# Kernel tuning notes

Measured on AMD Instinct MI355X. Metric: run time of the kernel, lower is better.

## Reference

```python
import jax, jax.numpy as jnp
import numpy as np
import math

HEAD_DIM = 64
RP_DIM = 256
B, H, N = 4, 8, 4096
EPS = 1e-4  # performer positive-feature epsilon


def _ortho_gaussian_matrix(m, d, seed=0):
    # gaussian_orthogonal_random_matrix, scaling=0: stack QR-orthogonalized
    # d x d gaussian blocks, scale rows by norms of an iid gaussian matrix.
    rng = np.random.default_rng(seed)
    blocks = []
    for _ in range(int(np.ceil(m / d))):
        g = rng.standard_normal((d, d))
        q, _ = np.linalg.qr(g)
        blocks.append(q.T)
    mat = np.concatenate(blocks, axis=0)[:m]
    multiplier = np.linalg.norm(rng.standard_normal((m, d)), axis=1)
    return (multiplier[:, None] * mat).astype(np.float32)


def _softmax_features(x, proj, is_query):
    # FAVOR+ positive random features: ratio * exp(Wx - ||x||^2/2 - stab) + eps
    ratio = proj.shape[0] ** -0.5
    xp = jnp.einsum('bhnd,md->bhnm', x, proj)
    diag = 0.5 * jnp.sum(x * x, axis=-1, keepdims=True)
    if is_query:
        stab = jnp.max(xp, axis=-1, keepdims=True)
    else:
        stab = jnp.max(xp, axis=(-1, -2), keepdims=True)
    return ratio * (jnp.exp(xp - diag - stab) + EPS)


def setup_inputs() -> dict:
    key = jax.random.key(0)
    kq, kk, kv = jax.random.split(key, 3)
    Q = jax.random.normal(kq, (B, H, N, HEAD_DIM), dtype=jnp.float32)
    K = jax.random.normal(kk, (B, H, N, HEAD_DIM), dtype=jnp.float32)
    V = jax.random.normal(kv, (B, H, N, HEAD_DIM), dtype=jnp.float32)
    mask = jnp.ones((B, N), dtype=jnp.float32)
    projection = jnp.asarray(_ortho_gaussian_matrix(RP_DIM, HEAD_DIM, seed=0))
    return {'Q': Q, 'K': K, 'V': V, 'mask': mask, 'projection': projection}


def reference(Q, K, V, mask, projection):
    scale = HEAD_DIM ** -0.25  # 1/sqrt(sqrt(head_dim))
    m = mask[:, None, :, None]
    q = Q * scale
    k = K * scale * m
    v = V * m
    phi_q = _softmax_features(q, projection, is_query=True)   # [b,h,n,m]
    phi_k = _softmax_features(k, projection, is_query=False)  # [b,h,n,m]
    # non-causal linear attention
    k_sum = jnp.sum(phi_k, axis=2)                                   # [b,h,m]
    D_inv = 1.0 / jnp.einsum('bhnm,bhm->bhn', phi_q, k_sum)          # [b,h,n]
    context = jnp.einsum('bhnm,bhne->bhme', phi_k, v)                # [b,h,m,e]
    out = jnp.einsum('bhme,bhnm,bhn->bhne', context, phi_q, D_inv)   # [b,h,n,e]
    return out
```

## Files before the change

kernel.cpp:

```cpp
#include <hip/hip_runtime.h>
#include <hip/hip_bf16.h>


typedef __attribute__((ext_vector_type(8))) short short8;
typedef __attribute__((ext_vector_type(4))) float floatx4;

constexpr int BB = 4, HH = 8, NN = 4096, DD = 64, MM = 256, BH = 32;
constexpr int NCH = 16;
constexpr float SCALE = 0.3535533905932738f;
constexpr float RATIO = 0.0625f;
constexpr float EPSI  = 1e-4f;
constexpr float NEGINF = -3.4e38f;

__device__ inline unsigned pk2(float a, float b) {
  unsigned ua = __float_as_uint(a) + 0x8000u;
  unsigned ub = __float_as_uint(b) + 0x8000u;
  return (ua >> 16) | (ub & 0xffff0000u);
}
__device__ inline float hif(float x) {
  return __uint_as_float((__float_as_uint(x) + 0x8000u) & 0xffff0000u);
}
__device__ inline unsigned short bhi(float x) {
  return (unsigned short)((__float_as_uint(x) + 0x8000u) >> 16);
}
__device__ inline int ph16(int i) { return (i & 56) | ((i + (i >> 3)) & 7); }

union Frag { short8 s8; unsigned u[4]; };

__device__ inline void atomicMaxF(float* a, float v) {
  unsigned* ai = (unsigned*)a;
  unsigned old = __atomic_load_n(ai, __ATOMIC_RELAXED);
  while (__uint_as_float(old) < v) {
    unsigned assumed = old;
    old = atomicCAS(ai, assumed, __float_as_uint(v));
    if (old == assumed) break;
  }
}

__global__ __launch_bounds__(256) void prep_kernel(
    const float* __restrict__ proj, unsigned short* __restrict__ projH,
    unsigned short* __restrict__ projL, float* __restrict__ stabk,
    float* __restrict__ Vs, float* __restrict__ ctxsum,
    float* __restrict__ ksE) {
  const int i = blockIdx.x * 256 + threadIdx.x;
  float v = proj[i];
  projH[i] = bhi(v);
  projL[i] = bhi(v - hif(v));
  if (i < BH) stabk[i] = NEGINF;
  if (i < 2048) { Vs[i] = 0.f; ctxsum[i] = 0.f; }
  if (i < 8192) ksE[i] = 0.f;
}

template <bool PARTIAL>
__global__ __launch_bounds__(256) void kside_kernel(
    const float* __restrict__ K, const float* __restrict__ V,
    const float* __restrict__ mask,
    const unsigned short* __restrict__ projH, const unsigned short* __restrict__ projL,
    float* __restrict__ stabk, float* __restrict__ ksE,
    float* __restrict__ ctxOut, float* __restrict__ Vs) {
  const int bh = blockIdx.y, b = bh >> 3;
  const int t = threadIdx.x;
  const int w = t >> 6, l = t & 63, c = l & 15, sq = l >> 4;
  const int m0 = w * 64;

  __shared__ __align__(16) unsigned short sK[2][32 * 72];
  __shared__ __align__(16) unsigned short sVt[2][64 * 40];
  __shared__ float sDiag[32];
  __shared__ float sRed[4];
  __shared__ float sVsum[4][64];
  __shared__ __align__(16) unsigned short sPhi[4][2][512];

  Frag Bp[4][2][2];
#pragma unroll
  for (int tt = 0; tt < 4; ++tt)
#pragma unroll
    for (int s = 0; s < 2; ++s) {
      const size_t o = (size_t)(m0 + tt * 16 + c) * DD + s * 32 + sq * 8;
      Bp[tt][s][0].s8 = *(const short8*)&projH[o];
      Bp[tt][s][1].s8 = *(const short8*)&projL[o];
    }

  floatx4 ctxacc[4][4];
#pragma unroll
  for (int i = 0; i < 4; ++i)
#pragma unroll
    for (int j = 0; j < 4; ++j) ctxacc[i][j] = (floatx4){0.f, 0.f, 0.f, 0.f};
  float ksac[4] = {0.f, 0.f, 0.f, 0.f};
  float mxloc = NEGINF;
  float vsacc = 0.f;

  const int r0 = blockIdx.x * 256;

  float4 pk4[2], pv4[2];
  float pmk[2], pmv[2];
  {
    const int rb = r0;
#pragma unroll
    for (int rep = 0; rep < 2; ++rep) {
      const int f = t + rep * 256;
      const int n = f >> 4;
      pmk[rep] = mask[b * NN + rb + n];
      pk4[rep] = *(const float4*)(K + ((size_t)bh * NN + rb + n) * DD + (f & 15) * 4);
      const int n_loc = w * 4 + rep * 16 + sq;
      pmv[rep] = mask[b * NN + rb + n_loc];
      pv4[rep] = *(const float4*)(V + ((size_t)bh * NN + rb + n_loc) * DD + c * 4);
    }
  }

  for (int ch = 0; ch < 8; ++ch) {
    __syncthreads();

#pragma unroll
    for (int rep = 0; rep < 2; ++rep) {
      const int f = t + rep * 256;
      const int n = f >> 4, dg = f & 15;
      const float msc = pmk[rep] * SCALE;
      float k0 = pk4[rep].x * msc, k1 = pk4[rep].y * msc,
            k2 = pk4[rep].z * msc, k3 = pk4[rep].w * msc;
      float ss = fmaf(k0, k0, fmaf(k1, k1, fmaf(k2, k2, k3 * k3)));
      ss += __shfl_xor(ss, 1); ss += __shfl_xor(ss, 2);
      ss += __shfl_xor(ss, 4); ss += __shfl_xor(ss, 8);
      if (dg == 0) sDiag[n] = 0.5f * ss;
      unsigned h0 = pk2(k0, k1), h1 = pk2(k2, k3);
      float q0 = k0 - hif(k0), q1 = k1 - hif(k1);
      float q2 = k2 - hif(k2), q3 = k3 - hif(k3);
      *(uint2*)(&sK[0][n * 72 + dg * 4]) = make_uint2(h0, h1);
      *(uint2*)(&sK[1][n * 72 + dg * 4]) = make_uint2(pk2(q0, q1), pk2(q2, q3));
    }

#pragma unroll
    for (int rep = 0; rep < 2; ++rep) {
      const int nb = w * 4 + rep * 16;
      const float mk = pmv[rep];
      float4 vv = pv4[rep];
      float va[4] = {vv.x * mk, vv.y * mk, vv.z * mk, vv.w * mk};
      float g[4];
#pragma unroll
      for (int k = 0; k < 4; ++k) {
        const int gi = (sq + k) & 3;
        float sel = va[(sq - k) & 3];
        g[gi] = __shfl(sel, gi * 16 + c);
      }
      const int estar = c * 4 + sq;
      vsacc += ((g[0] + g[1]) + (g[2] + g[3]));
      unsigned h0 = pk2(g[0], g[1]), h1 = pk2(g[2], g[3]);
      float q0 = g[0] - hif(g[0]), q1 = g[1] - hif(g[1]);
      float q2 = g[2] - hif(g[2]), q3 = g[3] - hif(g[3]);
      *(uint2*)(&sVt[0][estar * 40 + nb]) = make_uint2(h0, h1);
      *(uint2*)(&sVt[1][estar * 40 + nb]) = make_uint2(pk2(q0, q1), pk2(q2, q3));
    }
    __syncthreads();

    if (ch < 7) {
      const int rb = r0 + (ch + 1) * 32;
#pragma unroll
      for (int rep = 0; rep < 2; ++rep) {
        const int f = t + rep * 256;
        const int n = f >> 4;
        pmk[rep] = mask[b * NN + rb + n];
        pk4[rep] = *(const float4*)(K + ((size_t)bh * NN + rb + n) * DD + (f & 15) * 4);
        const int n_loc = w * 4 + rep * 16 + sq;
        pmv[rep] = mask[b * NN + rb + n_loc];
        pv4[rep] = *(const float4*)(V + ((size_t)bh * NN + rb + n_loc) * DD + c * 4);
      }
    }

    Frag Ak[2][2][2];
#pragma unroll
    for (int i = 0; i < 2; ++i)
#pragma unroll
      for (int s = 0; s < 2; ++s) {
        Ak[i][s][0].s8 = *(const short8*)&sK[0][(i * 16 + c) * 72 + s * 32 + sq * 8];
        Ak[i][s][1].s8 = *(const short8*)&sK[1][(i * 16 + c) * 72 + s * 32 + sq * 8];
      }
    Frag Bv[4][2];
#pragma unroll
    for (int E = 0; E < 4; ++E) {
      Bv[E][0].s8 = *(const short8*)&sVt[0][(E * 16 + c) * 40 + sq * 8];
      Bv[E][1].s8 = *(const short8*)&sVt[1][(E * 16 + c) * 40 + sq * 8];
    }

#pragma unroll
    for (int tt = 0; tt < 4; ++tt) {
      floatx4 xacc[2];
#pragma unroll
      for (int i = 0; i < 2; ++i) {
        floatx4 a = (floatx4){0.f, 0.f, 0.f, 0.f};
#pragma unroll
        for (int s = 0; s < 2; ++s) {
          a = __builtin_amdgcn_mfma_f32_16x16x32_bf16(Ak[i][s][0].s8, Bp[tt][s][0].s8, a, 0, 0, 0);
          a = __builtin_amdgcn_mfma_f32_16x16x32_bf16(Ak[i][s][0].s8, Bp[tt][s][1].s8, a, 0, 0, 0);
          a = __builtin_amdgcn_mfma_f32_16x16x32_bf16(Ak[i][s][1].s8, Bp[tt][s][0].s8, a, 0, 0, 0);
        }
        xacc[i] = a;
      }
      const int qp_c = sq >> 1, half = (sq & 1) * 4;
#pragma unroll
      for (int i = 0; i < 2; ++i) {
        float p[4];
#pragma unroll
        for (int jj = 0; jj < 4; ++jj) {
          float xp = xacc[i][jj];
          mxloc = fmaxf(mxloc, xp);
          p[jj] = __expf(xp - sDiag[i * 16 + sq * 4 + jj]);
          ksac[tt] += p[jj];
        }
        unsigned h0 = pk2(p[0], p[1]), h1 = pk2(p[2], p[3]);
        float q0 = p[0] - hif(p[0]), q1 = p[1] - hif(p[1]);
        float q2 = p[2] - hif(p[2]), q3 = p[3] - hif(p[3]);
        const int tl = (i * 2 + qp_c) * 16 + c;
        const int idx = ph16(tl) * 8 + half;
        *(uint2*)&sPhi[w][0][idx] = make_uint2(h0, h1);
        *(uint2*)&sPhi[w][1][idx] = make_uint2(pk2(q0, q1), pk2(q2, q3));
      }
      Frag Ap[2];
      Ap[0].s8 = *(const short8*)&sPhi[w][0][ph16(l) * 8];
      Ap[1].s8 = *(const short8*)&sPhi[w][1][ph16(l) * 8];
#pragma unroll
      for (int E = 0; E < 4; ++E) {
        ctxacc[tt][E] = __builtin_amdgcn_mfma_f32_16x16x32_bf16(Ap[0].s8, Bv[E][0].s8, ctxacc[tt][E], 0, 0, 0);
        ctxacc[tt][E] = __builtin_amdgcn_mfma_f32_16x16x32_bf16(Ap[0].s8, Bv[E][1].s8, ctxacc[tt][E], 0, 0, 0);
        ctxacc[tt][E] = __builtin_amdgcn_mfma_f32_16x16x32_bf16(Ap[1].s8, Bv[E][0].s8, ctxacc[tt][E], 0, 0, 0);
      }
    }
  }

#pragma unroll
  for (int tt = 0; tt < 4; ++tt) {
    float v = ksac[tt];
    v += __shfl_xor(v, 16);
    v += __shfl_xor(v, 32);
    if (sq == 0) atomicAdd(&ksE[bh * MM + m0 + tt * 16 + c], v);
  }
#pragma unroll
  for (int off = 1; off <= 32; off <<= 1) mxloc = fmaxf(mxloc, __shfl_xor(mxloc, off));
  if (l == 0) sRed[w] = mxloc;
  sVsum[w][c * 4 + sq] = vsacc;
  __syncthreads();
  if (t == 0)
    atomicMaxF(&stabk[bh], fmaxf(fmaxf(sRed[0], sRed[1]), fmaxf(sRed[2], sRed[3])));
  if (t < 64)
    atomicAdd(&Vs[bh * DD + t],
              (sVsum[0][t] + sVsum[1][t]) + (sVsum[2][t] + sVsum[3][t]));

  if (PARTIAL) {
    float* cg = ctxOut + ((size_t)(bh * NCH + blockIdx.x) * MM) * DD;
#pragma unroll
    for (int tt = 0; tt < 4; ++tt)
#pragma unroll
      for (int E = 0; E < 4; ++E)
#pragma unroll
        for (int r = 0; r < 4; ++r)
          cg[(m0 + tt * 16 + sq * 4 + r) * DD + E * 16 + c] = ctxacc[tt][E][r];
  } else {
    float* cg = ctxOut + (size_t)bh * MM * DD;
#pragma unroll
    for (int tt = 0; tt < 4; ++tt)
#pragma unroll
      for (int E = 0; E < 4; ++E)
#pragma unroll
        for (int r = 0; r < 4; ++r)
          atomicAdd(&cg[(m0 + tt * 16 + sq * 4 + r) * DD + E * 16 + c],
                    ctxacc[tt][E][r]);
  }
}

template <int NPARTS>
__global__ __launch_bounds__(256) void fixup_kernel(
    const float* __restrict__ stabk, const float* __restrict__ Vs,
    const float* __restrict__ ksE, const float* __restrict__ ctxParts,
    float* __restrict__ ksum, float* __restrict__ kssum,
    float* __restrict__ ctxsum, unsigned short* __restrict__ ctxTH,
    unsigned short* __restrict__ ctxTL) {
  const int bh = blockIdx.y, mc = blockIdx.x, t = threadIdx.x;
  const float es = __expf(-stabk[bh]);
  const int e = t & 63, g = t >> 6;
  const float vse = EPSI * Vs[bh * DD + e];

  __shared__ float tile[64 * 33];
  __shared__ float cred[256];

  float csum = 0.f;
#pragma unroll
  for (int r = 0; r < 8; ++r) {
    const int ml = r * 4 + g;
    const int m = mc * 32 + ml;
    float x = 0.f;
#pragma unroll
    for (int p = 0; p < NPARTS; ++p)
      x += ctxParts[(((size_t)bh * NPARTS + p) * MM + m) * DD + e];
    float v = RATIO * (es * x + vse);
    csum += v;
    tile[e * 33 + ml] = v;
  }
  cred[t] = csum;
  __syncthreads();
  if (t < 64)
    atomicAdd(&ctxsum[bh * DD + t],
              (cred[t] + cred[t + 64]) + (cred[t + 128] + cred[t + 192]));

  {
    const int ml5 = t & 31, elg = t >> 5;
#pragma unroll
    for (int r = 0; r < 8; ++r) {
      const int el = r * 8 + elg;
      float v = tile[el * 33 + ml5];
      const size_t o = ((size_t)(bh * DD + el)) * MM + mc * 32 + ml5;
      ctxTH[o] = bhi(v);
      ctxTL[o] = bhi(v - hif(v));
    }
  }

  if (mc == 0) {
    __syncthreads();
    const float kv = RATIO * (es * ksE[bh * MM + t] + (float)NN * EPSI);
    ksum[bh * MM + t] = kv;
    cred[t] = kv;
    __syncthreads();
    for (int off = 128; off >= 1; off >>= 1) {
      if (t < off) cred[t] += cred[t + off];
      __syncthreads();
    }
    if (t == 0) kssum[bh] = cred[0];
  }
}

__global__ __launch_bounds__(256, 2) void out_kernel(
    const float* __restrict__ Q,
    const unsigned short* __restrict__ projH, const unsigned short* __restrict__ projL,
    const float* __restrict__ ksum,
    const unsigned short* __restrict__ ctxTH, const unsigned short* __restrict__ ctxTL,
    const float* __restrict__ kssum, const float* __restrict__ ctxsum,
    float* __restrict__ out) {
  const int bh = blockIdx.y;
  const int r0 = blockIdx.x * 64;
  const int t = threadIdx.x, w = t >> 6, l = t & 63, c = l & 15, sq = l >> 4;

  __shared__ __align__(16) unsigned short sQ[2][64 * 80];
  __shared__ __align__(16) unsigned short sP[2][64 * 80];
  __shared__ __align__(16) unsigned short sC[2][64 * 80];
  __shared__ float sKs[256];
  __shared__ float sDiag[64];
  __shared__ __align__(16) unsigned short sPhi[4][2][2][512];

  {
    const int row = t >> 2, q4 = t & 3;
    const float* qp = Q + ((size_t)bh * NN + r0 + row) * DD + q4 * 16;
    float4 t0 = *(const float4*)(qp + 0), t1 = *(const float4*)(qp + 4),
           t2 = *(const float4*)(qp + 8), t3 = *(const float4*)(qp + 12);
    float v[16] = {t0.x, t0.y, t0.z, t0.w, t1.x, t1.y, t1.z, t1.w,
                   t2.x, t2.y, t2.z, t2.w, t3.x, t3.y, t3.z, t3.w};
    float ss = 0.f;
#pragma unroll
    for (int j = 0; j < 16; ++j) { v[j] *= SCALE; ss = fmaf(v[j], v[j], ss); }
    ss += __shfl_xor(ss, 1);
    ss += __shfl_xor(ss, 2);
    if (q4 == 0) sDiag[row] = 0.5f * ss;
    unsigned short* dh = &sQ[0][row * 80 + q4 * 16];
    unsigned short* dl = &sQ[1][row * 80 + q4 * 16];
#pragma unroll
    for (int j = 0; j < 8; ++j) {
      *(unsigned*)&dh[2 * j] = pk2(v[2 * j], v[2 * j + 1]);
      float l0 = v[2 * j] - hif(v[2 * j]), l1 = v[2 * j + 1] - hif(v[2 * j + 1]);
      *(unsigned*)&dl[2 * j] = pk2(l0, l1);
    }
  }
  sKs[t] = ksum[bh * MM + t];
  __syncthreads();

  Frag Bq[2][2];
#pragma unroll
  for (int s = 0; s < 2; ++s)
#pragma unroll
    for (int p = 0; p < 2; ++p)
      Bq[s][p].s8 = *(const short8*)&sQ[p][(w * 16 + c) * 80 + s * 32 + sq * 8];

  const float diagc = sDiag[w * 16 + c];
  floatx4 oacc[4];
#pragma unroll
  for (int E = 0; E < 4; ++E) oacc[E] = (floatx4){0.f, 0.f, 0.f, 0.f};
  float mxacc = NEGINF, dsacc = 0.f;

  for (int mc = 0; mc < 4; ++mc) {
    __syncthreads();
    {
      const int row = t >> 2, q4 = t & 3;
      const size_t gp = (size_t)(mc * 64 + row) * DD + q4 * 16;
      const uint4* ph = (const uint4*)&projH[gp];
      const uint4* pl = (const uint4*)&projL[gp];
      *(uint4*)&sP[0][row * 80 + q4 * 16] = ph[0];
      *(uint4*)&sP[0][row * 80 + q4 * 16 + 8] = ph[1];
      *(uint4*)&sP[1][row * 80 + q4 * 16] = pl[0];
      *(uint4*)&sP[1][row * 80 + q4 * 16 + 8] = pl[1];
      const size_t gc = ((size_t)bh * DD + row) * MM + mc * 64 + q4 * 16;
      const uint4* chh = (const uint4*)&ctxTH[gc];
      const uint4* cll = (const uint4*)&ctxTL[gc];
      *(uint4*)&sC[0][row * 80 + q4 * 16] = chh[0];
      *(uint4*)&sC[0][row * 80 + q4 * 16 + 8] = chh[1];
      *(uint4*)&sC[1][row * 80 + q4 * 16] = cll[0];
      *(uint4*)&sC[1][row * 80 + q4 * 16 + 8] = cll[1];
    }
    __syncthreads();

#pragma unroll
    for (int tt = 0; tt < 4; ++tt) {
      Frag Af[2][2];
#pragma unroll
      for (int s = 0; s < 2; ++s)
#pragma unroll
        for (int p = 0; p < 2; ++p)
          Af[s][p].s8 = *(const short8*)&sP[p][(tt * 16 + c) * 80 + s * 32 + sq * 8];
      floatx4 x = (floatx4){0.f, 0.f, 0.f, 0.f};
#pragma unroll
      for (int s = 0; s < 2; ++s) {
        x = __builtin_amdgcn_mfma_f32_16x16x32_bf16(Af[s][0].s8, Bq[s][0].s8, x, 0, 0, 0);
        x = __builtin_amdgcn_mfma_f32_16x16x32_bf16(Af[s][0].s8, Bq[s][1].s8, x, 0, 0, 0);
        x = __builtin_amdgcn_mfma_f32_16x16x32_bf16(Af[s][1].s8, Bq[s][0].s8, x, 0, 0, 0);
      }
      float p4[4];
#pragma unroll
      for (int jj = 0; jj < 4; ++jj) {
        const float xp = x[jj];
        mxacc = fmaxf(mxacc, xp);
        p4[jj] = __expf(xp - diagc);
        dsacc = fmaf(p4[jj], sKs[mc * 64 + tt * 16 + sq * 4 + jj], dsacc);
      }
      const int kstep = tt >> 1;
      const int tl = ((tt & 1) * 2 + (sq >> 1)) * 16 + c;
      const int off = (sq & 1) * 4;
      float l0 = p4[0] - hif(p4[0]), l1 = p4[1] - hif(p4[1]);
      float l2 = p4[2] - hif(p4[2]), l3 = p4[3] - hif(p4[3]);
      *(uint2*)&sPhi[w][0][kstep][tl * 8 + off] = make_uint2(pk2(p4[0], p4[1]), pk2(p4[2], p4[3]));
      *(uint2*)&sPhi[w][1][kstep][tl * 8 + off] = make_uint2(pk2(l0, l1), pk2(l2, l3));
    }

#pragma unroll
    for (int ks = 0; ks < 2; ++ks) {
      Frag Aph[2];
      Aph[0].s8 = *(const short8*)&sPhi[w][0][ks][l * 8];
      Aph[1].s8 = *(const short8*)&sPhi[w][1][ks][l * 8];
#pragma unroll
      for (int E = 0; E < 4; ++E) {
        Frag Bc0, Bc1;
        Bc0.s8 = *(const short8*)&sC[0][(E * 16 + c) * 80 + ks * 32 + sq * 8];
        Bc1.s8 = *(const short8*)&sC[1][(E * 16 + c) * 80 + ks * 32 + sq * 8];
        oacc[E] = __builtin_amdgcn_mfma_f32_16x16x32_bf16(Aph[0].s8, Bc0.s8, oacc[E], 0, 0, 0);
        oacc[E] = __builtin_amdgcn_mfma_f32_16x16x32_bf16(Aph[0].s8, Bc1.s8, oacc[E], 0, 0, 0);
        oacc[E] = __builtin_amdgcn_mfma_f32_16x16x32_bf16(Aph[1].s8, Bc0.s8, oacc[E], 0, 0, 0);
      }
    }
  }

  mxacc = fmaxf(mxacc, __shfl_xor(mxacc, 16));
  mxacc = fmaxf(mxacc, __shfl_xor(mxacc, 32));
  dsacc += __shfl_xor(dsacc, 16);
  dsacc += __shfl_xor(dsacc, 32);

  const float kss = kssum[bh];
  float fac[4], oinv[4];
#pragma unroll
  for (int jj = 0; jj < 4; ++jj) {
    const int src = sq * 4 + jj;
    const float s_row = __shfl(mxacc, src);
    const float d_row = __shfl(dsacc, src);
    const float f = __expf(s_row) * EPSI;
    fac[jj] = f;
    oinv[jj] = 1.f / (d_row + f * kss);
  }

  const float* csb = ctxsum + bh * DD;
#pragma unroll
  for (int E = 0; E < 4; ++E) {
    const float cse = csb[E * 16 + c];
#pragma unroll
    for (int jj = 0; jj < 4; ++jj) {
      const int row = r0 + w * 16 + sq * 4 + jj;
      out[((size_t)bh * NN + row) * DD + E * 16 + c] =
          (oacc[E][jj] + fac[jj] * cse) * oinv[jj];
    }
  }
}

extern "C" void kernel_launch(void* const* d_in, const int* in_sizes, int n_in,
                              void* d_out, int out_size, void* d_ws, size_t ws_size,
                              hipStream_t stream) {
  const float* Q    = (const float*)d_in[0];
  const float* K    = (const float*)d_in[1];
  const float* V    = (const float*)d_in[2];
  const float* mask = (const float*)d_in[3];
  const float* proj = (const float*)d_in[4];
  float* out = (float*)d_out;

  float* wsf = (float*)d_ws;
  float* stabk  = wsf;
  float* ksum   = wsf + 32;
  float* kssum  = wsf + 8224;
  float* Vs     = wsf + 8256;
  float* ctxsum = wsf + 10304;
  float* ksE    = wsf + 12352;
  unsigned short* projH = (unsigned short*)(wsf + 20544);
  unsigned short* projL = (unsigned short*)(wsf + 28736);
  unsigned short* ctxTH = (unsigned short*)(wsf + 36928);
  unsigned short* ctxTL = (unsigned short*)(wsf + 299072);
  float* ctxBig = wsf + 561216;

  const size_t need_partial = (size_t)(561216 + NCH * BH * MM * DD) * 4;
  const bool partial = ws_size >= need_partial;

  prep_kernel<<<64, 256, 0, stream>>>(proj, projH, projL, stabk, Vs, ctxsum, ksE);

  if (partial) {
    kside_kernel<true><<<dim3(NCH, BH), 256, 0, stream>>>(
        K, V, mask, projH, projL, stabk, ksE, ctxBig, Vs);
    fixup_kernel<NCH><<<dim3(8, BH), 256, 0, stream>>>(
        stabk, Vs, ksE, ctxBig, ksum, kssum, ctxsum, ctxTH, ctxTL);
  } else {
    hipMemsetAsync(ctxBig, 0, (size_t)MM * DD * BH * 4, stream);
    kside_kernel<false><<<dim3(NCH, BH), 256, 0, stream>>>(
        K, V, mask, projH, projL, stabk, ksE, ctxBig, Vs);
    fixup_kernel<1><<<dim3(8, BH), 256, 0, stream>>>(
        stabk, Vs, ksE, ctxBig, ksum, kssum, ctxsum, ctxTH, ctxTL);
  }

  out_kernel<<<dim3(64, BH), 256, 0, stream>>>(
      Q, projH, projL, ksum, ctxTH, ctxTL, kssum, ctxsum, out);
}
```

Baseline: 228.1 us.

## Stage projection and context tiles via global_load_lds DMA with XOR swizzle

Replaces the register round-trip loads of projection and context tiles in out_kernel with direct global-to-LDS loads (global_load_lds) into XOR-swizzled unpadded planes. The next chunk's tile is issued as soon as the current one has been consumed, so loads can overlap the remaining MFMA work. Q staging and the phi scratch share one LDS buffer to cut shared memory, and the launch-bounds occupancy hint is dropped. Relies on implicit completion at the following barrier for the DMA writes, which could be a correctness risk if the compiler does not insert the needed vmcnt waits.

```diff
diff --git a/kernel.cpp b/kernel.cpp
--- a/kernel.cpp
+++ b/kernel.cpp
@@ -11,6 +11,11 @@
 constexpr float RATIO = 0.0625f;
 constexpr float EPSI  = 1e-4f;
 constexpr float NEGINF = -3.4e38f;
+
+#define GLOAD_LDS16(SRC, DST)                                        \
+  __builtin_amdgcn_global_load_lds(                                  \
+      (const __attribute__((address_space(1))) unsigned int*)(SRC),  \
+      (__attribute__((address_space(3))) unsigned int*)(DST), 16, 0, 0)
 
 __device__ inline unsigned pk2(float a, float b) {
   unsigned ua = __float_as_uint(a) + 0x8000u;
@@ -325,7 +330,7 @@
   }
 }
 
-__global__ __launch_bounds__(256, 2) void out_kernel(
+__global__ __launch_bounds__(256) void out_kernel(
     const float* __restrict__ Q,
     const unsigned short* __restrict__ projH, const unsigned short* __restrict__ projL,
     const float* __restrict__ ksum,
@@ -335,16 +340,38 @@
   const int bh = blockIdx.y;
   const int r0 = blockIdx.x * 64;
   const int t = threadIdx.x, w = t >> 6, l = t & 63, c = l & 15, sq = l >> 4;
-
-  __shared__ __align__(16) unsigned short sQ[2][64 * 80];
-  __shared__ __align__(16) unsigned short sP[2][64 * 80];
-  __shared__ __align__(16) unsigned short sC[2][64 * 80];
+  const int row = t >> 2, q4 = t & 3;
+
+  __shared__ __align__(16) unsigned short sQPhi[8192];
+  __shared__ __align__(16) unsigned short sP[2][4096];
+  __shared__ __align__(16) unsigned short sC[2][4096];
   __shared__ float sKs[256];
   __shared__ float sDiag[64];
-  __shared__ __align__(16) unsigned short sPhi[4][2][2][512];
+#define SQ_(p, idx) sQPhi[(p) * 4096 + (idx)]
+#define SPHI_(wv, p, ks, idx) sQPhi[((((wv) * 2 + (p)) * 2 + (ks)) * 512) + (idx)]
+
+  const unsigned short* ctxH_b = ctxTH + (size_t)bh * DD * MM;
+  const unsigned short* ctxL_b = ctxTL + (size_t)bh * DD * MM;
+
+  auto stageDMA = [&](const unsigned short* srcBase, int rowStride,
+                      unsigned short* plane) {
+#pragma unroll
+    for (int r2 = 0; r2 < 2; ++r2) {
+      const int pc = r2 * 256 + t;
+      const int prow = pc >> 3, pch4 = pc & 7;
+      const int lch4 = pch4 ^ (prow & 7);
+      const unsigned short* src = srcBase + prow * rowStride + lch4 * 8;
+      unsigned short* dst = plane + (r2 * 256 + (t & 192)) * 8;
+      GLOAD_LDS16(src, dst);
+    }
+  };
+
+  stageDMA(projH, DD, &sP[0][0]);
+  stageDMA(projL, DD, &sP[1][0]);
+  stageDMA(ctxH_b, MM, &sC[0][0]);
+  stageDMA(ctxL_b, MM, &sC[1][0]);
 
   {
-    const int row = t >> 2, q4 = t & 3;
     const float* qp = Q + ((size_t)bh * NN + r0 + row) * DD + q4 * 16;
     float4 t0 = *(const float4*)(qp + 0), t1 = *(const float4*)(qp + 4),
            t2 = *(const float4*)(qp + 8), t3 = *(const float4*)(qp + 12);
@@ -356,8 +383,8 @@
     ss += __shfl_xor(ss, 1);
     ss += __shfl_xor(ss, 2);
     if (q4 == 0) sDiag[row] = 0.5f * ss;
-    unsigned short* dh = &sQ[0][row * 80 + q4 * 16];
-    unsigned short* dl = &sQ[1][row * 80 + q4 * 16];
+    unsigned short* dh = &SQ_(0, row * 64 + q4 * 16);
+    unsigned short* dl = &SQ_(1, row * 64 + q4 * 16);
 #pragma unroll
     for (int j = 0; j < 8; ++j) {
       *(unsigned*)&dh[2 * j] = pk2(v[2 * j], v[2 * j + 1]);
@@ -373,43 +400,25 @@
   for (int s = 0; s < 2; ++s)
 #pragma unroll
     for (int p = 0; p < 2; ++p)
-      Bq[s][p].s8 = *(const short8*)&sQ[p][(w * 16 + c) * 80 + s * 32 + sq * 8];
-
+      Bq[s][p].s8 = *(const short8*)&SQ_(p, (w * 16 + c) * 64 + s * 32 + sq * 8);
   const float diagc = sDiag[w * 16 + c];
+  __syncthreads();
+
   floatx4 oacc[4];
 #pragma unroll
   for (int E = 0; E < 4; ++E) oacc[E] = (floatx4){0.f, 0.f, 0.f, 0.f};
   float mxacc = NEGINF, dsacc = 0.f;
 
   for (int mc = 0; mc < 4; ++mc) {
-    __syncthreads();
-    {
-      const int row = t >> 2, q4 = t & 3;
-      const size_t gp = (size_t)(mc * 64 + row) * DD + q4 * 16;
-      const uint4* ph = (const uint4*)&projH[gp];
-      const uint4* pl = (const uint4*)&projL[gp];
-      *(uint4*)&sP[0][row * 80 + q4 * 16] = ph[0];
-      *(uint4*)&sP[0][row * 80 + q4 * 16 + 8] = ph[1];
-      *(uint4*)&sP[1][row * 80 + q4 * 16] = pl[0];
-      *(uint4*)&sP[1][row * 80 + q4 * 16 + 8] = pl[1];
-      const size_t gc = ((size_t)bh * DD + row) * MM + mc * 64 + q4 * 16;
-      const uint4* chh = (const uint4*)&ctxTH[gc];
-      const uint4* cll = (const uint4*)&ctxTL[gc];
-      *(uint4*)&sC[0][row * 80 + q4 * 16] = chh[0];
-      *(uint4*)&sC[0][row * 80 + q4 * 16 + 8] = chh[1];
-      *(uint4*)&sC[1][row * 80 + q4 * 16] = cll[0];
-      *(uint4*)&sC[1][row * 80 + q4 * 16 + 8] = cll[1];
-    }
-    __syncthreads();
-
 #pragma unroll
     for (int tt = 0; tt < 4; ++tt) {
       Frag Af[2][2];
 #pragma unroll
-      for (int s = 0; s < 2; ++s)
-#pragma unroll
-        for (int p = 0; p < 2; ++p)
-          Af[s][p].s8 = *(const short8*)&sP[p][(tt * 16 + c) * 80 + s * 32 + sq * 8];
+      for (int s = 0; s < 2; ++s) {
+        const int a = (tt * 16 + c) * 64 + (((s * 4 + sq) ^ (c & 7)) * 8);
+        Af[s][0].s8 = *(const short8*)&sP[0][a];
+        Af[s][1].s8 = *(const short8*)&sP[1][a];
+      }
       floatx4 x = (floatx4){0.f, 0.f, 0.f, 0.f};
 #pragma unroll
       for (int s = 0; s < 2; ++s) {
@@ -430,26 +439,41 @@
       const int off = (sq & 1) * 4;
       float l0 = p4[0] - hif(p4[0]), l1 = p4[1] - hif(p4[1]);
       float l2 = p4[2] - hif(p4[2]), l3 = p4[3] - hif(p4[3]);
-      *(uint2*)&sPhi[w][0][kstep][tl * 8 + off] = make_uint2(pk2(p4[0], p4[1]), pk2(p4[2], p4[3]));
-      *(uint2*)&sPhi[w][1][kstep][tl * 8 + off] = make_uint2(pk2(l0, l1), pk2(l2, l3));
+      *(uint2*)&SPHI_(w, 0, kstep, tl * 8 + off) = make_uint2(pk2(p4[0], p4[1]), pk2(p4[2], p4[3]));
+      *(uint2*)&SPHI_(w, 1, kstep, tl * 8 + off) = make_uint2(pk2(l0, l1), pk2(l2, l3));
+    }
+
+    __syncthreads();
+    if (mc < 3) {
+      stageDMA(projH + (mc + 1) * 64 * DD, DD, &sP[0][0]);
+      stageDMA(projL + (mc + 1) * 64 * DD, DD, &sP[1][0]);
     }
 
 #pragma unroll
     for (int ks = 0; ks < 2; ++ks) {
       Frag Aph[2];
-      Aph[0].s8 = *(const short8*)&sPhi[w][0][ks][l * 8];
-      Aph[1].s8 = *(const short8*)&sPhi[w][1][ks][l * 8];
+      Aph[0].s8 = *(const short8*)&SPHI_(w, 0, ks, l * 8);
+      Aph[1].s8 = *(const short8*)&SPHI_(w, 1, ks, l * 8);
 #pragma unroll
       for (int E = 0; E < 4; ++E) {
+        const int a = (E * 16 + c) * 64 + (((ks * 4 + sq) ^ (c & 7)) * 8);
         Frag Bc0, Bc1;
-        Bc0.s8 = *(const short8*)&sC[0][(E * 16 + c) * 80 + ks * 32 + sq * 8];
-        Bc1.s8 = *(const short8*)&sC[1][(E * 16 + c) * 80 + ks * 32 + sq * 8];
+        Bc0.s8 = *(const short8*)&sC[0][a];
+        Bc1.s8 = *(const short8*)&sC[1][a];
         oacc[E] = __builtin_amdgcn_mfma_f32_16x16x32_bf16(Aph[0].s8, Bc0.s8, oacc[E], 0, 0, 0);
         oacc[E] = __builtin_amdgcn_mfma_f32_16x16x32_bf16(Aph[0].s8, Bc1.s8, oacc[E], 0, 0, 0);
         oacc[E] = __builtin_amdgcn_mfma_f32_16x16x32_bf16(Aph[1].s8, Bc0.s8, oacc[E], 0, 0, 0);
       }
     }
-  }
+
+    __syncthreads();
+    if (mc < 3) {
+      stageDMA(ctxH_b + (mc + 1) * 64, MM, &sC[0][0]);
+      stageDMA(ctxL_b + (mc + 1) * 64, MM, &sC[1][0]);
+    }
+  }
+#undef SQ_
+#undef SPHI_
 
   mxacc = fmaxf(mxacc, __shfl_xor(mxacc, 16));
   mxacc = fmaxf(mxacc, __shfl_xor(mxacc, 32));
@@ -474,8 +498,8 @@
     const float cse = csb[E * 16 + c];
 #pragma unroll
     for (int jj = 0; jj < 4; ++jj) {
-      const int row = r0 + w * 16 + sq * 4 + jj;
-      out[((size_t)bh * NN + row) * DD + E * 16 + c] =
+      const int row2 = r0 + w * 16 + sq * 4 + jj;
+      out[((size_t)bh * NN + row2) * DD + E * 16 + c] =
           (oacc[E][jj] + fac[jj] * cse) * oinv[jj];
     }
   }
```

After: 254.8 us. 11.7% more time.
